# Kernel tuning notes

Measured on AMD Instinct MI355X. Metric: run time of the kernel, lower is better.

Reference implementation:

```python
import jax, jax.numpy as jnp
import numpy as np

VOCAB = 32000
PAD = 0
E = 256   # EMBEDDING_DIM
H = 512   # HIDDEN_SIZE
B = 64
S = 512


def setup_inputs() -> dict:
    key = jax.random.key(0)
    k_tok, k_len, k_emb, k_wi, k_wh, k_bi, k_bh = jax.random.split(key, 7)
    tokens = jax.random.randint(k_tok, (B, S), 1, VOCAB)  # non-pad ids
    lengths = jax.random.randint(k_len, (B,), 1, S + 1)
    mask = jnp.arange(S)[None, :] < lengths[:, None]      # right-padded
    x = jnp.where(mask, tokens, PAD).astype(jnp.int64)
    s = 1.0 / np.sqrt(H)
    emb = jax.random.normal(k_emb, (VOCAB, E), dtype=jnp.float32)
    emb = emb.at[PAD].set(0.0)  # padding_idx row is zero
    W_ih = jax.random.uniform(k_wi, (3 * H, E), minval=-s, maxval=s, dtype=jnp.float32)
    W_hh = jax.random.uniform(k_wh, (3 * H, H), minval=-s, maxval=s, dtype=jnp.float32)
    b_ih = jax.random.uniform(k_bi, (3 * H,), minval=-s, maxval=s, dtype=jnp.float32)
    b_hh = jax.random.uniform(k_bh, (3 * H,), minval=-s, maxval=s, dtype=jnp.float32)
    return {"x": x, "emb": emb, "W_ih": W_ih, "W_hh": W_hh, "b_ih": b_ih, "b_hh": b_hh}


def _gru_encode(x, emb, W_ih, W_hh, b_ih, b_hh):
    ex = emb[x]                                           # [B,S,E]
    # precompute input projections for all timesteps (one big GEMM)
    gi = jnp.einsum('bse,ge->bsg', ex, W_ih) + b_ih       # [B,S,3H]
    gi = jnp.transpose(gi, (1, 0, 2))                     # [S,B,3H]

    def step(h, gi_t):
        gh = h @ W_hh.T + b_hh                            # [B,3H]
        i_r, i_z, i_n = jnp.split(gi_t, 3, axis=-1)
        h_r, h_z, h_n = jnp.split(gh, 3, axis=-1)
        r = jax.nn.sigmoid(i_r + h_r)
        z = jax.nn.sigmoid(i_z + h_z)
        n = jnp.tanh(i_n + r * h_n)
        h_new = (1.0 - z) * n + z * h
        return h_new, h_new

    h0 = jnp.zeros((x.shape[0], W_hh.shape[1]), dtype=emb.dtype)
    _, outputs = jax.lax.scan(step, h0, gi)               # [S,B,H]
    lengths = (x != PAD).sum(axis=1)                      # [B]
    last = outputs[lengths - 1, jnp.arange(x.shape[0])]   # [B,H]
    return last


def reference(x, emb, W_ih, W_hh, b_ih, b_hh):
    return _gru_encode(x, emb, W_ih, W_hh, b_ih, b_hh)
```

## Files before the change

kernel.cpp:

```cpp
#include <hip/hip_runtime.h>
#include <stdint.h>

#define B_  64
#define S_  512
#define E_  256
#define H_  512

typedef float  f32x4  __attribute__((ext_vector_type(4)));
typedef __bf16 bf16x8 __attribute__((ext_vector_type(8)));
typedef unsigned long long u64t;

__device__ __forceinline__ unsigned short f2b(float f) {
  uint32_t u = __builtin_bit_cast(uint32_t, f);
  uint32_t r = (u + 0x7FFFu + ((u >> 16) & 1u)) >> 16;
  return (unsigned short)r;
}
__device__ __forceinline__ float b2f(unsigned short s) {
  uint32_t u = ((uint32_t)s) << 16;
  return __builtin_bit_cast(float, u);
}
__device__ __forceinline__ bf16x8 ld_bf8(const unsigned short* p) {
  uint4 v = *reinterpret_cast<const uint4*>(p);
  return __builtin_bit_cast(bf16x8, v);
}

__global__ void convert_kernel(const float* __restrict__ emb,
                               const float* __restrict__ wih,
                               unsigned short* __restrict__ emb_b,
                               unsigned short* __restrict__ wih_b) {
  const int64_t EMB_N = (int64_t)32000 * 256;
  const int64_t TOT8  = (EMB_N + (int64_t)1536 * 256) / 8;
  for (int64_t i8 = (int64_t)blockIdx.x * blockDim.x + threadIdx.x; i8 < TOT8;
       i8 += (int64_t)gridDim.x * blockDim.x) {
    int64_t e = i8 * 8;
    const float* src; unsigned short* dst;
    if (e < EMB_N) { src = emb + e;           dst = emb_b + e; }
    else           { src = wih + (e - EMB_N); dst = wih_b + (e - EMB_N); }
    float4 a = *reinterpret_cast<const float4*>(src);
    float4 b = *reinterpret_cast<const float4*>(src + 4);
    uint4 o;
    o.x = (unsigned)f2b(a.x) | ((unsigned)f2b(a.y) << 16);
    o.y = (unsigned)f2b(a.z) | ((unsigned)f2b(a.w) << 16);
    o.z = (unsigned)f2b(b.x) | ((unsigned)f2b(b.y) << 16);
    o.w = (unsigned)f2b(b.z) | ((unsigned)f2b(b.w) << 16);
    *reinterpret_cast<uint4*>(dst) = o;
  }
}

__global__ void lengths_kernel(const int* __restrict__ x, int* __restrict__ len) {
  __shared__ int part[8];
  int b = blockIdx.x, tid = threadIdx.x;
  int v = (x[b * S_ + tid] != 0) ? 1 : 0;
  unsigned long long m = __ballot(v);
  if ((tid & 63) == 0) part[tid >> 6] = __popcll(m);
  __syncthreads();
  if (tid == 0) {
    int s = 0;
    #pragma unroll
    for (int i = 0; i < 8; ++i) s += part[i];
    len[b] = s;
  }
}

__global__ void init_kernel(u64t* __restrict__ x64) {
  int i = blockIdx.x * blockDim.x + threadIdx.x;
  u64t v = (i < 16384) ? 0ull : 0xFFFFFFFF00000000ull;
  __hip_atomic_store(x64 + i, v, __ATOMIC_RELAXED, __HIP_MEMORY_SCOPE_AGENT);
}

__global__ __launch_bounds__(256) void gi_kernel(
    const int* __restrict__ x, const unsigned short* __restrict__ emb_b,
    const unsigned short* __restrict__ wih_b, const float* __restrict__ b_ih,
    unsigned short* __restrict__ gi) {
  int tblk = blockIdx.x, g = blockIdx.y, w = blockIdx.z;
  int tid = threadIdx.x;
  int wv = tid >> 6, lane = tid & 63;
  int c16 = lane & 15, kq = lane >> 4;
  int t0 = tblk * 8 + wv, t1 = t0 + 4;

  int grow[6]; float bias[6];
  #pragma unroll
  for (int nt = 0; nt < 6; ++nt) {
    grow[nt] = (nt >> 1) * H_ + w * 32 + (nt & 1) * 16 + c16;
    bias[nt] = b_ih[grow[nt]];
  }
  int tok0 = x[(g * 16 + c16) * S_ + t0];
  int tok1 = x[(g * 16 + c16) * S_ + t1];

  f32x4 acc[2][6];
  #pragma unroll
  for (int nt = 0; nt < 6; ++nt) {
    acc[0][nt] = f32x4{bias[nt], bias[nt], bias[nt], bias[nt]};
    acc[1][nt] = acc[0][nt];
  }
  #pragma unroll
  for (int kk = 0; kk < 8; ++kk) {
    int kb = kk * 32 + kq * 8;
    bf16x8 A0 = ld_bf8(emb_b + (size_t)tok0 * E_ + kb);
    bf16x8 A1 = ld_bf8(emb_b + (size_t)tok1 * E_ + kb);
    #pragma unroll
    for (int nt = 0; nt < 6; ++nt) {
      bf16x8 Bf = ld_bf8(wih_b + (size_t)grow[nt] * E_ + kb);
      acc[0][nt] = __builtin_amdgcn_mfma_f32_16x16x32_bf16(A0, Bf, acc[0][nt], 0, 0, 0);
      acc[1][nt] = __builtin_amdgcn_mfma_f32_16x16x32_bf16(A1, Bf, acc[1][nt], 0, 0, 0);
    }
  }
  int wg = g * 16 + w;
  #pragma unroll
  for (int m = 0; m < 2; ++m) {
    int t = m ? t1 : t0;
    size_t base = ((size_t)(t * 64 + wg) * 16) * 96;
    #pragma unroll
    for (int nt = 0; nt < 6; ++nt)
      #pragma unroll
      for (int j = 0; j < 4; ++j)
        gi[base + (size_t)(kq * 4 + j) * 96 + nt * 16 + c16] = f2b(acc[m][nt][j]);
  }
}

__global__ __launch_bounds__(768, 1) void scan_kernel(
    const float* __restrict__ whh, const float* __restrict__ b_hh,
    const unsigned short* __restrict__ gi, const int* __restrict__ len,
    u64t* __restrict__ xchg64, float* __restrict__ out) {
  __shared__ float gh[2][16 * 100];
  __shared__ float hown[16 * 32];
  __shared__ uint4 frag4[2][1024];

  const int wgid = blockIdx.x, g = wgid >> 4, w = wgid & 15;
  const int tid = threadIdx.x, wv = tid >> 6, lane = tid & 63;
  const int nt = wv % 6, kh = wv / 6;
  const int c16 = lane & 15, kq = lane >> 4;

  const int grow = (nt >> 1) * H_ + w * 32 + (nt & 1) * 16 + c16;
  bf16x8 Bf[8];
  #pragma unroll
  for (int kk = 0; kk < 8; ++kk) {
    int kb = kh * 256 + kk * 32 + kq * 8;
    const float* p = whh + (size_t)grow * H_ + kb;
    float4 a = *reinterpret_cast<const float4*>(p);
    float4 b = *reinterpret_cast<const float4*>(p + 4);
    uint4 v;
    v.x = (unsigned)f2b(a.x) | ((unsigned)f2b(a.y) << 16);
    v.y = (unsigned)f2b(a.z) | ((unsigned)f2b(a.w) << 16);
    v.z = (unsigned)f2b(b.x) | ((unsigned)f2b(b.y) << 16);
    v.w = (unsigned)f2b(b.z) | ((unsigned)f2b(b.w) << 16);
    Bf[kk] = __builtin_bit_cast(bf16x8, v);
  }
  const float bhh_v = (kh == 0) ? b_hh[grow] : 0.0f;

  if (tid < 512) hown[tid] = 0.0f;
  const int i_e = (tid >> 5) & 15, c_e = tid & 31;
  const int lenv = len[g * 16 + i_e];
  int tmax = 0;
  for (int bi = 0; bi < 16; ++bi) {
    int l = len[g * 16 + bi];
    tmax = l > tmax ? l : tmax;
  }

  const int prow = lane & 15, pcolrun = wv * 4 + (lane >> 4);
  const int pkh = pcolrun >> 3, pkk = pcolrun & 7;
  __syncthreads();

  for (int t = 0; t < tmax; ++t) {
    const int p = t & 1;
    size_t gib = ((size_t)(t * 64 + wgid) * 16 + i_e) * 96;
    float i_r = b2f(gi[gib + c_e]);
    float i_z = b2f(gi[gib + 32 + c_e]);
    float i_n = b2f(gi[gib + 64 + c_e]);

    if (wv < 4) {
      const char* pb = reinterpret_cast<const char*>(
          xchg64 + (size_t)((p * 4 + g) * 16 + prow) * 256 + pcolrun * 16);
      const uint32_t etag = (uint32_t)t;
      uint4 L[8];
      bool ok = false;
      int s = 0;
      while (!ok && ++s < (1 << 16)) {
        #pragma unroll
        for (int i = 0; i < 8; ++i)
          asm volatile("global_load_dwordx4 %0, %1, off sc0 sc1"
                       : "=v"(L[i]) : "v"(pb + i * 16) : "memory");
        asm volatile("s_waitcnt vmcnt(0)" ::: "memory");
        ok = true;
        #pragma unroll
        for (int i = 0; i < 8; ++i)
          ok = ok & (L[i].y == etag) & (L[i].w == etag);
      }
      #pragma unroll
      for (int q = 0; q < 4; ++q)
        frag4[p][((pkh * 8 + pkk) * 4 + q) * 16 + prow] =
            uint4{L[2 * q].x, L[2 * q].z, L[2 * q + 1].x, L[2 * q + 1].z};
    }
    __syncthreads();

    f32x4 acc = f32x4{bhh_v, bhh_v, bhh_v, bhh_v};
    #pragma unroll
    for (int kk = 0; kk < 8; ++kk) {
      uint4 af = frag4[p][((kh * 8 + kk) * 4 + kq) * 16 + c16];
      acc = __builtin_amdgcn_mfma_f32_16x16x32_bf16(
          __builtin_bit_cast(bf16x8, af), Bf[kk], acc, 0, 0, 0);
    }
    float* ghp = gh[kh];
    #pragma unroll
    for (int j = 0; j < 4; ++j)
      ghp[(kq * 4 + j) * 100 + nt * 16 + c16] = acc[j];
    __syncthreads();

    if (tid < 512) {
      float gr_ = gh[0][i_e * 100 + c_e]      + gh[1][i_e * 100 + c_e];
      float gz_ = gh[0][i_e * 100 + 32 + c_e] + gh[1][i_e * 100 + 32 + c_e];
      float gn_ = gh[0][i_e * 100 + 64 + c_e] + gh[1][i_e * 100 + 64 + c_e];
      float hp = hown[i_e * 32 + c_e];
      float r = 1.0f / (1.0f + __expf(-(i_r + gr_)));
      float z = 1.0f / (1.0f + __expf(-(i_z + gz_)));
      float pre = i_n + r * gn_;
      float e2 = __expf(2.0f * pre);
      float n = 1.0f - 2.0f / (e2 + 1.0f);
      float hn = z * (hp - n) + n;
      hown[i_e * 32 + c_e] = hn;
      unsigned short hb = f2b(hn);
      unsigned nb = (unsigned)__shfl_down((int)hb, 1) & 0xFFFFu;
      if ((c_e & 1) == 0) {
        u64t pack = ((u64t)(uint32_t)(t + 1) << 32) | ((u64t)nb << 16) | hb;
        u64t* dst = xchg64 + (size_t)((((t + 1) & 1) * 4 + g) * 16 + i_e) * 256 +
                    w * 16 + (c_e >> 1);
        __hip_atomic_store(dst, pack, __ATOMIC_RELAXED,
                           __HIP_MEMORY_SCOPE_AGENT);
      }
      if (t + 1 == lenv) out[(size_t)(g * 16 + i_e) * H_ + w * 32 + c_e] = hn;
    }
  }
}

extern "C" void kernel_launch(void* const* d_in, const int* in_sizes, int n_in,
                              void* d_out, int out_size, void* d_ws, size_t ws_size,
                              hipStream_t stream) {
  const int*   x    = (const int*)d_in[0];
  const float* emb  = (const float*)d_in[1];
  const float* wih  = (const float*)d_in[2];
  const float* whh  = (const float*)d_in[3];
  const float* b_ih = (const float*)d_in[4];
  const float* b_hh = (const float*)d_in[5];
  float* out = (float*)d_out;

  char* ws = (char*)d_ws;
  const size_t GI_SZ    = (size_t)512 * 64 * 16 * 96 * 2;
  const size_t EMB_SZ   = (size_t)32000 * 256 * 2;
  const size_t WIH_SZ   = (size_t)1536 * 256 * 2;
  const size_t XCHG_SZ  = (size_t)32768 * 8;
  const size_t LEN_SZ   = 256;
  const size_t GI_OFF   = 0;
  const size_t EMB_OFF  = GI_OFF + GI_SZ;
  const size_t WIH_OFF  = EMB_OFF + EMB_SZ;
  const size_t XCHG_OFF = WIH_OFF + WIH_SZ;
  const size_t LEN_OFF  = XCHG_OFF + XCHG_SZ;
  if (ws_size < LEN_OFF + LEN_SZ) return;

  unsigned short* gi_p  = (unsigned short*)(ws + GI_OFF);
  unsigned short* emb_b = (unsigned short*)(ws + EMB_OFF);
  unsigned short* wih_b = (unsigned short*)(ws + WIH_OFF);
  u64t*           xchg  = (u64t*)(ws + XCHG_OFF);
  int*            len   = (int*)(ws + LEN_OFF);

  init_kernel<<<128, 256, 0, stream>>>(xchg);
  convert_kernel<<<2048, 256, 0, stream>>>(emb, wih, emb_b, wih_b);
  lengths_kernel<<<64, 512, 0, stream>>>(x, len);
  gi_kernel<<<dim3(64, 4, 16), 256, 0, stream>>>(x, emb_b, wih_b, b_ih, gi_p);
  scan_kernel<<<64, 768, 0, stream>>>(whh, b_hh, gi_p, len, xchg, out);
}
```

Before: 2.957 ms.

## Move exchange polling to idle waves with double-buffered atomic loads

Polling of the cross-workgroup hidden-state exchange buffer moves from waves 0-3 to waves 8+, which do not run the elementwise gate update, and the gi loads are now limited to threads that use them. The spin loop swaps the asm cache-bypassing dwordx4 loads for 64-bit relaxed agent-scope atomic loads and keeps two batches of loads in flight, so the next poll is already issued while the previous one is checked. The wave-wide check uses __all. The aim is to cut handoff latency per timestep in the serial recurrence. The cost is more load instructions per poll (16 64-bit loads instead of 8 128-bit), and the code assumes the block has at least 12 waves.

```diff
diff --git a/kernel.cpp b/kernel.cpp
--- a/kernel.cpp
+++ b/kernel.cpp
@@ -157,39 +157,57 @@
     tmax = l > tmax ? l : tmax;
   }
 
-  const int prow = lane & 15, pcolrun = wv * 4 + (lane >> 4);
-  const int pkh = pcolrun >> 3, pkk = pcolrun & 7;
+  const int prow = lane & 15, pcolrun = (wv - 8) * 4 + (lane >> 4);
+  const int fbase = pcolrun * 4;
   __syncthreads();
 
   for (int t = 0; t < tmax; ++t) {
     const int p = t & 1;
-    size_t gib = ((size_t)(t * 64 + wgid) * 16 + i_e) * 96;
-    float i_r = b2f(gi[gib + c_e]);
-    float i_z = b2f(gi[gib + 32 + c_e]);
-    float i_n = b2f(gi[gib + 64 + c_e]);
-
-    if (wv < 4) {
-      const char* pb = reinterpret_cast<const char*>(
-          xchg64 + (size_t)((p * 4 + g) * 16 + prow) * 256 + pcolrun * 16);
+    float i_r = 0.f, i_z = 0.f, i_n = 0.f;
+    if (tid < 512) {
+      size_t gib = ((size_t)(t * 64 + wgid) * 16 + i_e) * 96;
+      i_r = b2f(gi[gib + c_e]);
+      i_z = b2f(gi[gib + 32 + c_e]);
+      i_n = b2f(gi[gib + 64 + c_e]);
+    }
+
+    if (wv >= 8) {
+      const u64t* pw = xchg64 + (size_t)((p * 4 + g) * 16 + prow) * 256 +
+                       pcolrun * 16;
       const uint32_t etag = (uint32_t)t;
-      uint4 L[8];
-      bool ok = false;
+      u64t A[16], Bv[16];
+      #pragma unroll
+      for (int j = 0; j < 16; ++j)
+        A[j] = __hip_atomic_load(pw + j, __ATOMIC_RELAXED,
+                                 __HIP_MEMORY_SCOPE_AGENT);
+      bool useA = true;
       int s = 0;
-      while (!ok && ++s < (1 << 16)) {
-        #pragma unroll
-        for (int i = 0; i < 8; ++i)
-          asm volatile("global_load_dwordx4 %0, %1, off sc0 sc1"
-                       : "=v"(L[i]) : "v"(pb + i * 16) : "memory");
-        asm volatile("s_waitcnt vmcnt(0)" ::: "memory");
+      for (;;) {
+        #pragma unroll
+        for (int j = 0; j < 16; ++j)
+          Bv[j] = __hip_atomic_load(pw + j, __ATOMIC_RELAXED,
+                                    __HIP_MEMORY_SCOPE_AGENT);
+        bool ok = true;
+        #pragma unroll
+        for (int j = 0; j < 16; ++j) ok &= ((uint32_t)(A[j] >> 32) == etag);
+        if (__all(ok) || ++s >= (1 << 16)) { useA = true; break; }
+        #pragma unroll
+        for (int j = 0; j < 16; ++j)
+          A[j] = __hip_atomic_load(pw + j, __ATOMIC_RELAXED,
+                                   __HIP_MEMORY_SCOPE_AGENT);
         ok = true;
         #pragma unroll
-        for (int i = 0; i < 8; ++i)
-          ok = ok & (L[i].y == etag) & (L[i].w == etag);
+        for (int j = 0; j < 16; ++j) ok &= ((uint32_t)(Bv[j] >> 32) == etag);
+        if (__all(ok) || ++s >= (1 << 16)) { useA = false; break; }
       }
       #pragma unroll
-      for (int q = 0; q < 4; ++q)
-        frag4[p][((pkh * 8 + pkk) * 4 + q) * 16 + prow] =
-            uint4{L[2 * q].x, L[2 * q].z, L[2 * q + 1].x, L[2 * q + 1].z};
+      for (int q = 0; q < 4; ++q) {
+        uint4 fa = uint4{(uint32_t)A[4 * q],     (uint32_t)A[4 * q + 1],
+                         (uint32_t)A[4 * q + 2], (uint32_t)A[4 * q + 3]};
+        uint4 fb = uint4{(uint32_t)Bv[4 * q],     (uint32_t)Bv[4 * q + 1],
+                         (uint32_t)Bv[4 * q + 2], (uint32_t)Bv[4 * q + 3]};
+        frag4[p][(fbase + q) * 16 + prow] = useA ? fa : fb;
+      }
     }
     __syncthreads();
 
```

New measurement: 4.568 ms. 1.54x slower.
